# Kernel tuning notes

Measured on AMD Instinct MI355X. Metric: run time of the kernel, lower is better.

The kernel has to match this reference:

```python
import jax, jax.numpy as jnp
import numpy as np


def _entropy(x):
    # x: [..., C]; rowwise entropy of softmax(x) along last axis
    logp = jax.nn.log_softmax(x, axis=-1)
    return -(jnp.exp(logp) * logp).sum(-1)


def setup_inputs() -> dict:
    key = jax.random.key(0)
    C, E = 8192, 512
    prototypes = jax.random.normal(key, (C, E), dtype=jnp.float32)
    return {"prototypes": prototypes}


def reference(prototypes):
    C, E = prototypes.shape
    # F.normalize(p=2, dim=1): divide by L2 norm clamped to 1e-12
    norm = jnp.sqrt(jnp.sum(prototypes * prototypes, axis=1, keepdims=True))
    p = prototypes / jnp.maximum(norm, 1e-12)
    # Gram matrix [C, C] (fused matmul instead of broadcast-mul-sum)
    proto_logits = jnp.einsum("ce,de->cd", p, p)
    proto_logits_sum = proto_logits.sum(0, keepdims=True)  # [1, C]
    loss = _entropy(proto_logits).sum(-1) / C + _entropy(proto_logits_sum)
    return loss.sum()
```

## Files before the change

### kernel.cpp

```cpp
#include <hip/hip_runtime.h>
#include <hip/hip_bf16.h>

#define C_DIM 8192
#define E_DIM 512

using f32x4 = __attribute__((ext_vector_type(4))) float;
using i32x4 = __attribute__((ext_vector_type(4))) int;

__device__ inline void gload_lds16(const void* g, void* l) {
  __builtin_amdgcn_global_load_lds(
      (const __attribute__((address_space(1))) unsigned*)g,
      (__attribute__((address_space(3))) unsigned*)l, 16, 0, 0);
}

__device__ inline unsigned pack_bf16(float a, float b) {
  unsigned ua = __float_as_uint(a), ub = __float_as_uint(b);
  ua = (ua + 0x7fffu + ((ua >> 16) & 1u)) >> 16;
  ub = (ub + 0x7fffu + ((ub >> 16) & 1u)) >> 16;
  return ua | (ub << 16);
}

__device__ inline float bf2f(unsigned short u) {
  return __uint_as_float(((unsigned)u) << 16);
}

__device__ inline unsigned pack_i8x4(float a, float b, float c, float d) {
  unsigned x0 = (unsigned)(__float2int_rn(a * 127.f)) & 255u;
  unsigned x1 = (unsigned)(__float2int_rn(b * 127.f)) & 255u;
  unsigned x2 = (unsigned)(__float2int_rn(c * 127.f)) & 255u;
  unsigned x3 = (unsigned)(__float2int_rn(d * 127.f)) & 255u;
  return x0 | (x1 << 8) | (x2 << 16) | (x3 << 24);
}

__global__ __launch_bounds__(256) void norm_kernel(
    const float* __restrict__ P, unsigned* __restrict__ Pb,
    unsigned* __restrict__ Pi) {
  int wid = threadIdx.x >> 6, lane = threadIdx.x & 63;
  int row = blockIdx.x * 4 + wid;
  const float4* src = (const float4*)(P + (size_t)row * E_DIM);
  float4 v0 = src[lane], v1 = src[lane + 64];
  float ss = v0.x * v0.x + v0.y * v0.y + v0.z * v0.z + v0.w * v0.w +
             v1.x * v1.x + v1.y * v1.y + v1.z * v1.z + v1.w * v1.w;
  for (int m = 32; m; m >>= 1) ss += __shfl_xor(ss, m);
  float inv = 1.0f / fmaxf(sqrtf(ss), 1e-12f);
  v0.x *= inv; v0.y *= inv; v0.z *= inv; v0.w *= inv;
  v1.x *= inv; v1.y *= inv; v1.z *= inv; v1.w *= inv;
  uint2* bd = (uint2*)(Pb + (size_t)row * (E_DIM / 2));
  uint2 b0, b1;
  b0.x = pack_bf16(v0.x, v0.y); b0.y = pack_bf16(v0.z, v0.w);
  b1.x = pack_bf16(v1.x, v1.y); b1.y = pack_bf16(v1.z, v1.w);
  bd[lane] = b0; bd[lane + 64] = b1;
  Pi[(size_t)row * 128 + lane] = pack_i8x4(v0.x, v0.y, v0.z, v0.w);
  Pi[(size_t)row * 128 + 64 + lane] = pack_i8x4(v1.x, v1.y, v1.z, v1.w);
}

__global__ __launch_bounds__(256) void qsum_kernel(
    const unsigned short* __restrict__ Pb, float* __restrict__ q) {
  __shared__ float red[4][512];
  int wid = threadIdx.x >> 6, lane = threadIdx.x & 63;
  float a[8];
#pragma unroll
  for (int k = 0; k < 8; ++k) a[k] = 0.f;
  for (int i = 0; i < 32; ++i) {
    int row = blockIdx.x * 128 + wid * 32 + i;
    uint4 v = *(const uint4*)(Pb + (size_t)row * E_DIM + lane * 8);
    a[0] += bf2f((unsigned short)(v.x & 0xffff));
    a[1] += bf2f((unsigned short)(v.x >> 16));
    a[2] += bf2f((unsigned short)(v.y & 0xffff));
    a[3] += bf2f((unsigned short)(v.y >> 16));
    a[4] += bf2f((unsigned short)(v.z & 0xffff));
    a[5] += bf2f((unsigned short)(v.z >> 16));
    a[6] += bf2f((unsigned short)(v.w & 0xffff));
    a[7] += bf2f((unsigned short)(v.w >> 16));
  }
#pragma unroll
  for (int k = 0; k < 8; ++k) red[wid][lane * 8 + k] = a[k];
  __syncthreads();
  for (int c = threadIdx.x; c < 512; c += 256) {
    float t = red[0][c] + red[1][c] + red[2][c] + red[3][c];
    atomicAdd(&q[c], t);
  }
}

__global__ __launch_bounds__(256) void ssum_kernel(
    const unsigned short* __restrict__ Pb, const float* __restrict__ q,
    float* __restrict__ s) {
  int wid = threadIdx.x >> 6, lane = threadIdx.x & 63;
  int row = blockIdx.x * 4 + wid;
  uint4 v = *(const uint4*)(Pb + (size_t)row * E_DIM + lane * 8);
  const float4* qv = (const float4*)q;
  float4 q0 = qv[lane * 2], q1 = qv[lane * 2 + 1];
  float d = bf2f((unsigned short)(v.x & 0xffff)) * q0.x +
            bf2f((unsigned short)(v.x >> 16)) * q0.y +
            bf2f((unsigned short)(v.y & 0xffff)) * q0.z +
            bf2f((unsigned short)(v.y >> 16)) * q0.w +
            bf2f((unsigned short)(v.z & 0xffff)) * q1.x +
            bf2f((unsigned short)(v.z >> 16)) * q1.y +
            bf2f((unsigned short)(v.w & 0xffff)) * q1.z +
            bf2f((unsigned short)(v.w >> 16)) * q1.w;
  for (int m = 32; m; m >>= 1) d += __shfl_xor(d, m);
  if (lane == 0) s[row] = d;
}

__global__ __launch_bounds__(256) void gram_kernel(
    const unsigned char* __restrict__ Pi, float* __restrict__ Zp,
    float* __restrict__ Sp) {
  __shared__ unsigned char As[128 * 128];
  __shared__ unsigned char Bs[128 * 128];

  int b = blockIdx.x;
  int i = (b & 7) * 260 + (b >> 3);
  float bi = 64.5f - sqrtf(64.5f * 64.5f - 2.0f * (float)i);
  int by = (int)bi;
  if (by < 0) by = 0;
  while (64 * (by + 1) - ((by + 1) * by) / 2 <= i) ++by;
  while (64 * by - (by * (by - 1)) / 2 > i) --by;
  int bx = by + (i - (64 * by - (by * (by - 1)) / 2));
  bool diag = (bx == by);

  int tid = threadIdx.x, wid = tid >> 6, lane = tid & 63;
  int wr = wid >> 1, wc = wid & 1;
  int l15 = lane & 15, lh = lane >> 4;

  i32x4 acc[4][4];
#pragma unroll
  for (int m = 0; m < 4; ++m)
#pragma unroll
    for (int n = 0; n < 4; ++n)
      acc[m][n] = (i32x4){0, 0, 0, 0};

  int rs = lane >> 3;
  int gsw = (lane & 7) ^ rs;
  const unsigned char* abase = Pi + (size_t)(by * 128) * E_DIM;
  const unsigned char* bbase = Pi + (size_t)(bx * 128) * E_DIM;

  for (int kt = 0; kt < 4; ++kt) {
#pragma unroll
    for (int j = 0; j < 4; ++j) {
      int ci = wid * 4 + j;
      int r = ci * 8 + rs;
      gload_lds16(abase + (size_t)r * E_DIM + kt * 128 + gsw * 16,
                  (char*)As + ci * 1024);
      gload_lds16(bbase + (size_t)r * E_DIM + kt * 128 + gsw * 16,
                  (char*)Bs + ci * 1024);
    }
    __syncthreads();

    i32x4 af[4][2], bfr[4][2];
#pragma unroll
    for (int m = 0; m < 4; ++m)
#pragma unroll
      for (int kk = 0; kk < 2; ++kk) {
        int row = wr * 64 + m * 16 + l15;
        int g = (kk * 4 + lh) ^ (row & 7);
        af[m][kk] = *(const i32x4*)(As + row * 128 + g * 16);
      }
#pragma unroll
    for (int n = 0; n < 4; ++n)
#pragma unroll
      for (int kk = 0; kk < 2; ++kk) {
        int row = wc * 64 + n * 16 + l15;
        int g = (kk * 4 + lh) ^ (row & 7);
        bfr[n][kk] = *(const i32x4*)(Bs + row * 128 + g * 16);
      }

#pragma unroll
    for (int kk = 0; kk < 2; ++kk)
#pragma unroll
      for (int m = 0; m < 4; ++m)
#pragma unroll
        for (int n = 0; n < 4; ++n)
          acc[m][n] = __builtin_amdgcn_mfma_i32_16x16x64_i8(
              af[m][kk], bfr[n][kk], acc[m][n], 0, 0, 0);
    if (kt < 3) __syncthreads();
  }

  const float invq = 1.0f / 16129.0f;
  float zc[4], sc[4];
#pragma unroll
  for (int n = 0; n < 4; ++n) { zc[n] = 0.f; sc[n] = 0.f; }

  int slotR = bx * 2 + wc;
#pragma unroll
  for (int m = 0; m < 4; ++m) {
#pragma unroll
    for (int reg = 0; reg < 4; ++reg) {
      float z = 0.f, s = 0.f;
#pragma unroll
      for (int n = 0; n < 4; ++n) {
        float g = (float)acc[m][n][reg] * invq;
        float e = __expf(g);
        z += e;
        s += e * g;
        zc[n] += e;
        sc[n] += e * g;
      }
      for (int msk = 8; msk; msk >>= 1) {
        z += __shfl_xor(z, msk);
        s += __shfl_xor(s, msk);
      }
      if (l15 == 0) {
        int rowin = wr * 64 + m * 16 + lh * 4 + reg;
        size_t idx = (size_t)by * 16384 + (size_t)slotR * 128 + rowin;
        Zp[idx] = z;
        Sp[idx] = s;
      }
    }
  }
  if (!diag) {
    int slotC = by * 2 + wr;
#pragma unroll
    for (int n = 0; n < 4; ++n) {
      float z = zc[n], s = sc[n];
      z += __shfl_xor(z, 16); s += __shfl_xor(s, 16);
      z += __shfl_xor(z, 32); s += __shfl_xor(s, 32);
      if (lh == 0) {
        int colin = wc * 64 + n * 16 + l15;
        size_t idx = (size_t)bx * 16384 + (size_t)slotC * 128 + colin;
        Zp[idx] = z;
        Sp[idx] = s;
      }
    }
  }
}

__global__ __launch_bounds__(256) void reduce_kernel(
    const float* __restrict__ Zp, const float* __restrict__ Sp,
    const float* __restrict__ s, float* __restrict__ h_acc,
    unsigned* __restrict__ done, float* __restrict__ out) {
  __shared__ float zbuf[128], sbuf[128];
  __shared__ float red[8];
  __shared__ unsigned lastFlag;
  int rb = blockIdx.x;
  int t = threadIdx.x;
  int lane = t & 63, wid = t >> 6;
  int row = t & 127;
  const float* src = (t >= 128) ? Sp : Zp;
  size_t base = (size_t)rb * 16384 + row;
  float acc = 0.f;
#pragma unroll 8
  for (int sl = 0; sl < 128; ++sl) acc += src[base + (size_t)sl * 128];
  if (t >= 128) sbuf[row] = acc; else zbuf[row] = acc;
  __syncthreads();

  float hp = 0.f;
  if (t < 128) {
    float z = zbuf[t], s2 = sbuf[t];
    hp = logf(z) - s2 / z;
  }
  for (int k = 32; k; k >>= 1) hp += __shfl_xor(hp, k);
  if (lane == 0) red[wid] = hp;
  __syncthreads();
  if (t == 0) {
    float h = red[0] + red[1];
    atomicAdd(h_acc, h);
    __threadfence();
    unsigned old = atomicAdd(done, 1u);
    lastFlag = (old == 63u) ? 1u : 0u;
  }
  __syncthreads();

  if (lastFlag) {
    float m = -3.4e38f;
    for (int i = t; i < C_DIM; i += 256) m = fmaxf(m, s[i]);
    for (int k = 32; k; k >>= 1) m = fmaxf(m, __shfl_xor(m, k));
    if (lane == 0) red[wid] = m;
    __syncthreads();
    m = fmaxf(fmaxf(red[0], red[1]), fmaxf(red[2], red[3]));

    float z = 0.f, sw = 0.f;
    for (int i = t; i < C_DIM; i += 256) {
      float tv = s[i] - m;
      float e = __expf(tv);
      z += e;
      sw += e * tv;
    }
    for (int k = 32; k; k >>= 1) {
      z += __shfl_xor(z, k);
      sw += __shfl_xor(sw, k);
    }
    __syncthreads();
    if (lane == 0) { red[wid] = z; red[4 + wid] = sw; }
    __syncthreads();
    if (t == 0) {
      float zt = red[0] + red[1] + red[2] + red[3];
      float st = red[4] + red[5] + red[6] + red[7];
      float H2 = logf(zt) - st / zt;
      float h = atomicAdd(h_acc, 0.0f);
      out[0] = h / (float)C_DIM + H2;
    }
  }
}

extern "C" void kernel_launch(void* const* d_in, const int* in_sizes, int n_in,
                              void* d_out, int out_size, void* d_ws, size_t ws_size,
                              hipStream_t stream) {
  const float* P = (const float*)d_in[0];
  float* out = (float*)d_out;

  char* ws = (char*)d_ws;
  unsigned* Pb = (unsigned*)ws;
  unsigned* Pi = (unsigned*)(ws + ((size_t)8 << 20));
  float* Zp = (float*)(ws + ((size_t)12 << 20));
  float* Sp = (float*)(ws + ((size_t)16 << 20));
  float* q = (float*)(ws + ((size_t)20 << 20));
  float* h_acc = (float*)(ws + ((size_t)20 << 20) + 2048);
  unsigned* done = (unsigned*)(ws + ((size_t)20 << 20) + 2052);
  float* s = (float*)(ws + ((size_t)20 << 20) + 4096);

  hipMemsetAsync(q, 0, 2056, stream);

  norm_kernel<<<C_DIM / 4, 256, 0, stream>>>(P, Pb, Pi);
  qsum_kernel<<<C_DIM / 128, 256, 0, stream>>>((const unsigned short*)Pb, q);
  ssum_kernel<<<C_DIM / 4, 256, 0, stream>>>((const unsigned short*)Pb, q, s);
  gram_kernel<<<2080, 256, 0, stream>>>((const unsigned char*)Pi, Zp, Sp);
  reduce_kernel<<<64, 256, 0, stream>>>(Zp, Sp, s, h_acc, done, out);
}
```

Measured before the change: 86.58 us.

## Fuse normalize, column-sum and row-dot prep kernels with grid barrier

Replaces the three preprocessing kernels (normalize with bf16/int8 output, column sum q, row dot s) with one persistent prep kernel of 256 blocks. Each block keeps its 32 normalized fp32 rows in LDS, atomically accumulates q, waits at a global atomic counter barrier, then computes s from LDS. This removes the bf16 intermediate buffer, its write and two re-reads, plus two kernel launches. In exchange it depends on all 256 blocks being co-resident for the spin barrier, and the large LDS footprint limits occupancy.

```diff
diff --git a/kernel.cpp b/kernel.cpp
--- a/kernel.cpp
+++ b/kernel.cpp
@@ -11,17 +11,6 @@
   __builtin_amdgcn_global_load_lds(
       (const __attribute__((address_space(1))) unsigned*)g,
       (__attribute__((address_space(3))) unsigned*)l, 16, 0, 0);
-}
-
-__device__ inline unsigned pack_bf16(float a, float b) {
-  unsigned ua = __float_as_uint(a), ub = __float_as_uint(b);
-  ua = (ua + 0x7fffu + ((ua >> 16) & 1u)) >> 16;
-  ub = (ub + 0x7fffu + ((ub >> 16) & 1u)) >> 16;
-  return ua | (ub << 16);
-}
-
-__device__ inline float bf2f(unsigned short u) {
-  return __uint_as_float(((unsigned)u) << 16);
 }
 
 __device__ inline unsigned pack_i8x4(float a, float b, float c, float d) {
@@ -32,74 +21,74 @@
   return x0 | (x1 << 8) | (x2 << 16) | (x3 << 24);
 }
 
-__global__ __launch_bounds__(256) void norm_kernel(
-    const float* __restrict__ P, unsigned* __restrict__ Pb,
-    unsigned* __restrict__ Pi) {
+__global__ __launch_bounds__(256) void prep_kernel(
+    const float* __restrict__ P, unsigned* __restrict__ Pi,
+    float* __restrict__ q, unsigned* __restrict__ qdone,
+    float* __restrict__ s) {
+  __shared__ float rows[32][512];
+  __shared__ float qpart[4][512];
+  __shared__ float qs[512];
   int wid = threadIdx.x >> 6, lane = threadIdx.x & 63;
-  int row = blockIdx.x * 4 + wid;
-  const float4* src = (const float4*)(P + (size_t)row * E_DIM);
-  float4 v0 = src[lane], v1 = src[lane + 64];
-  float ss = v0.x * v0.x + v0.y * v0.y + v0.z * v0.z + v0.w * v0.w +
-             v1.x * v1.x + v1.y * v1.y + v1.z * v1.z + v1.w * v1.w;
-  for (int m = 32; m; m >>= 1) ss += __shfl_xor(ss, m);
-  float inv = 1.0f / fmaxf(sqrtf(ss), 1e-12f);
-  v0.x *= inv; v0.y *= inv; v0.z *= inv; v0.w *= inv;
-  v1.x *= inv; v1.y *= inv; v1.z *= inv; v1.w *= inv;
-  uint2* bd = (uint2*)(Pb + (size_t)row * (E_DIM / 2));
-  uint2 b0, b1;
-  b0.x = pack_bf16(v0.x, v0.y); b0.y = pack_bf16(v0.z, v0.w);
-  b1.x = pack_bf16(v1.x, v1.y); b1.y = pack_bf16(v1.z, v1.w);
-  bd[lane] = b0; bd[lane + 64] = b1;
-  Pi[(size_t)row * 128 + lane] = pack_i8x4(v0.x, v0.y, v0.z, v0.w);
-  Pi[(size_t)row * 128 + 64 + lane] = pack_i8x4(v1.x, v1.y, v1.z, v1.w);
-}
-
-__global__ __launch_bounds__(256) void qsum_kernel(
-    const unsigned short* __restrict__ Pb, float* __restrict__ q) {
-  __shared__ float red[4][512];
-  int wid = threadIdx.x >> 6, lane = threadIdx.x & 63;
-  float a[8];
-#pragma unroll
-  for (int k = 0; k < 8; ++k) a[k] = 0.f;
-  for (int i = 0; i < 32; ++i) {
-    int row = blockIdx.x * 128 + wid * 32 + i;
-    uint4 v = *(const uint4*)(Pb + (size_t)row * E_DIM + lane * 8);
-    a[0] += bf2f((unsigned short)(v.x & 0xffff));
-    a[1] += bf2f((unsigned short)(v.x >> 16));
-    a[2] += bf2f((unsigned short)(v.y & 0xffff));
-    a[3] += bf2f((unsigned short)(v.y >> 16));
-    a[4] += bf2f((unsigned short)(v.z & 0xffff));
-    a[5] += bf2f((unsigned short)(v.z >> 16));
-    a[6] += bf2f((unsigned short)(v.w & 0xffff));
-    a[7] += bf2f((unsigned short)(v.w >> 16));
-  }
-#pragma unroll
-  for (int k = 0; k < 8; ++k) red[wid][lane * 8 + k] = a[k];
+  int rbase = blockIdx.x * 32;
+
+  float c0[8];
+#pragma unroll
+  for (int k = 0; k < 8; ++k) c0[k] = 0.f;
+
+  for (int r8 = 0; r8 < 8; ++r8) {
+    int rloc = wid * 8 + r8;
+    int row = rbase + rloc;
+    const float4* src = (const float4*)(P + (size_t)row * E_DIM);
+    float4 v0 = src[lane], v1 = src[lane + 64];
+    float ss = v0.x * v0.x + v0.y * v0.y + v0.z * v0.z + v0.w * v0.w +
+               v1.x * v1.x + v1.y * v1.y + v1.z * v1.z + v1.w * v1.w;
+    for (int m = 32; m; m >>= 1) ss += __shfl_xor(ss, m);
+    float inv = 1.0f / fmaxf(sqrtf(ss), 1e-12f);
+    v0.x *= inv; v0.y *= inv; v0.z *= inv; v0.w *= inv;
+    v1.x *= inv; v1.y *= inv; v1.z *= inv; v1.w *= inv;
+    *(float4*)&rows[rloc][lane * 4] = v0;
+    *(float4*)&rows[rloc][256 + lane * 4] = v1;
+    Pi[(size_t)row * 128 + lane] = pack_i8x4(v0.x, v0.y, v0.z, v0.w);
+    Pi[(size_t)row * 128 + 64 + lane] = pack_i8x4(v1.x, v1.y, v1.z, v1.w);
+    c0[0] += v0.x; c0[1] += v0.y; c0[2] += v0.z; c0[3] += v0.w;
+    c0[4] += v1.x; c0[5] += v1.y; c0[6] += v1.z; c0[7] += v1.w;
+  }
+#pragma unroll
+  for (int k = 0; k < 4; ++k) {
+    qpart[wid][lane * 4 + k] = c0[k];
+    qpart[wid][256 + lane * 4 + k] = c0[4 + k];
+  }
   __syncthreads();
   for (int c = threadIdx.x; c < 512; c += 256) {
-    float t = red[0][c] + red[1][c] + red[2][c] + red[3][c];
+    float t = qpart[0][c] + qpart[1][c] + qpart[2][c] + qpart[3][c];
     atomicAdd(&q[c], t);
   }
-}
-
-__global__ __launch_bounds__(256) void ssum_kernel(
-    const unsigned short* __restrict__ Pb, const float* __restrict__ q,
-    float* __restrict__ s) {
-  int wid = threadIdx.x >> 6, lane = threadIdx.x & 63;
-  int row = blockIdx.x * 4 + wid;
-  uint4 v = *(const uint4*)(Pb + (size_t)row * E_DIM + lane * 8);
-  const float4* qv = (const float4*)q;
-  float4 q0 = qv[lane * 2], q1 = qv[lane * 2 + 1];
-  float d = bf2f((unsigned short)(v.x & 0xffff)) * q0.x +
-            bf2f((unsigned short)(v.x >> 16)) * q0.y +
-            bf2f((unsigned short)(v.y & 0xffff)) * q0.z +
-            bf2f((unsigned short)(v.y >> 16)) * q0.w +
-            bf2f((unsigned short)(v.z & 0xffff)) * q1.x +
-            bf2f((unsigned short)(v.z >> 16)) * q1.y +
-            bf2f((unsigned short)(v.w & 0xffff)) * q1.z +
-            bf2f((unsigned short)(v.w >> 16)) * q1.w;
-  for (int m = 32; m; m >>= 1) d += __shfl_xor(d, m);
-  if (lane == 0) s[row] = d;
+  __syncthreads();
+
+  if (threadIdx.x == 0) {
+    __threadfence();
+    __hip_atomic_fetch_add(qdone, 1u, __ATOMIC_RELEASE, __HIP_MEMORY_SCOPE_AGENT);
+    while (__hip_atomic_load(qdone, __ATOMIC_ACQUIRE, __HIP_MEMORY_SCOPE_AGENT) <
+           256u)
+      __builtin_amdgcn_s_sleep(2);
+  }
+  __syncthreads();
+
+  for (int c = threadIdx.x; c < 512; c += 256)
+    qs[c] = __hip_atomic_load(&q[c], __ATOMIC_RELAXED, __HIP_MEMORY_SCOPE_AGENT);
+  __syncthreads();
+
+  for (int r8 = 0; r8 < 8; ++r8) {
+    int rloc = wid * 8 + r8;
+    float4 a0 = *(const float4*)&rows[rloc][lane * 4];
+    float4 a1 = *(const float4*)&rows[rloc][256 + lane * 4];
+    float4 q0 = *(const float4*)&qs[lane * 4];
+    float4 q1 = *(const float4*)&qs[256 + lane * 4];
+    float d = a0.x * q0.x + a0.y * q0.y + a0.z * q0.z + a0.w * q0.w +
+              a1.x * q1.x + a1.y * q1.y + a1.z * q1.z + a1.w * q1.w;
+    for (int m = 32; m; m >>= 1) d += __shfl_xor(d, m);
+    if (lane == 0) s[rbase + rloc] = d;
+  }
 }
 
 __global__ __launch_bounds__(256) void gram_kernel(
@@ -299,20 +288,18 @@
   float* out = (float*)d_out;
 
   char* ws = (char*)d_ws;
-  unsigned* Pb = (unsigned*)ws;
-  unsigned* Pi = (unsigned*)(ws + ((size_t)8 << 20));
-  float* Zp = (float*)(ws + ((size_t)12 << 20));
-  float* Sp = (float*)(ws + ((size_t)16 << 20));
-  float* q = (float*)(ws + ((size_t)20 << 20));
-  float* h_acc = (float*)(ws + ((size_t)20 << 20) + 2048);
-  unsigned* done = (unsigned*)(ws + ((size_t)20 << 20) + 2052);
-  float* s = (float*)(ws + ((size_t)20 << 20) + 4096);
-
-  hipMemsetAsync(q, 0, 2056, stream);
-
-  norm_kernel<<<C_DIM / 4, 256, 0, stream>>>(P, Pb, Pi);
-  qsum_kernel<<<C_DIM / 128, 256, 0, stream>>>((const unsigned short*)Pb, q);
-  ssum_kernel<<<C_DIM / 4, 256, 0, stream>>>((const unsigned short*)Pb, q, s);
+  unsigned* Pi = (unsigned*)ws;
+  float* Zp = (float*)(ws + ((size_t)4 << 20));
+  float* Sp = (float*)(ws + ((size_t)8 << 20));
+  float* q = (float*)(ws + ((size_t)12 << 20));
+  float* h_acc = (float*)(ws + ((size_t)12 << 20) + 2048);
+  unsigned* done = (unsigned*)(ws + ((size_t)12 << 20) + 2052);
+  unsigned* qdone = (unsigned*)(ws + ((size_t)12 << 20) + 2056);
+  float* s = (float*)(ws + ((size_t)12 << 20) + 4096);
+
+  hipMemsetAsync(q, 0, 2060, stream);
+
+  prep_kernel<<<256, 256, 0, stream>>>(P, Pi, q, qdone, s);
   gram_kernel<<<2080, 256, 0, stream>>>((const unsigned char*)Pi, Zp, Sp);
   reduce_kernel<<<64, 256, 0, stream>>>(Zp, Sp, s, h_acc, done, out);
 }
```

New measurement: 105.2 us. +21.5%, slower.

## Load B fragments directly from global, stage only A in LDS with wider tiles

Applied to the files above, without the earlier changes.

Drops the B-tile LDS buffer and loads B operand fragments straight from global memory into registers. A is staged in LDS in two 256-byte-wide K halves, so there are fewer barrier rounds (two instead of four) and no LDS traffic for B. The cost is uncoalesced per-lane global loads for B, which rely on L2/cache hits and may expose memory latency without LDS staging.

```diff
diff --git a/kernel.cpp b/kernel.cpp
--- a/kernel.cpp
+++ b/kernel.cpp
@@ -105,8 +105,7 @@
 __global__ __launch_bounds__(256) void gram_kernel(
     const unsigned char* __restrict__ Pi, float* __restrict__ Zp,
     float* __restrict__ Sp) {
-  __shared__ unsigned char As[128 * 128];
-  __shared__ unsigned char Bs[128 * 128];
+  __shared__ unsigned char As[128 * 256];
 
   int b = blockIdx.x;
   int i = (b & 7) * 260 + (b >> 3);
@@ -129,50 +128,54 @@
     for (int n = 0; n < 4; ++n)
       acc[m][n] = (i32x4){0, 0, 0, 0};
 
-  int rs = lane >> 3;
-  int gsw = (lane & 7) ^ rs;
   const unsigned char* abase = Pi + (size_t)(by * 128) * E_DIM;
-  const unsigned char* bbase = Pi + (size_t)(bx * 128) * E_DIM;
-
-  for (int kt = 0; kt < 4; ++kt) {
-#pragma unroll
-    for (int j = 0; j < 4; ++j) {
-      int ci = wid * 4 + j;
-      int r = ci * 8 + rs;
-      gload_lds16(abase + (size_t)r * E_DIM + kt * 128 + gsw * 16,
+  const unsigned char* bb[4];
+#pragma unroll
+  for (int n = 0; n < 4; ++n)
+    bb[n] = Pi + (size_t)(bx * 128 + wc * 64 + n * 16 + l15) * E_DIM + lh * 16;
+
+  int rs = lane >> 4;
+  int g = lane & 15;
+
+#pragma unroll
+  for (int h = 0; h < 2; ++h) {
+    if (h) __syncthreads();
+#pragma unroll
+    for (int j = 0; j < 8; ++j) {
+      int ci = wid * 8 + j;
+      int r = ci * 4 + rs;
+      int srcg = (g & 8) | ((g & 7) ^ (r & 7));
+      gload_lds16(abase + (size_t)r * E_DIM + h * 256 + srcg * 16,
                   (char*)As + ci * 1024);
-      gload_lds16(bbase + (size_t)r * E_DIM + kt * 128 + gsw * 16,
-                  (char*)Bs + ci * 1024);
     }
     __syncthreads();
 
-    i32x4 af[4][2], bfr[4][2];
-#pragma unroll
-    for (int m = 0; m < 4; ++m)
+#pragma unroll
+    for (int kt2 = 0; kt2 < 2; ++kt2) {
+      int kt = h * 2 + kt2;
+      i32x4 bfr[2][4];
+#pragma unroll
+      for (int kk = 0; kk < 2; ++kk)
+#pragma unroll
+        for (int n = 0; n < 4; ++n)
+          bfr[kk][n] = *(const i32x4*)(bb[n] + kt * 128 + kk * 64);
 #pragma unroll
       for (int kk = 0; kk < 2; ++kk) {
-        int row = wr * 64 + m * 16 + l15;
-        int g = (kk * 4 + lh) ^ (row & 7);
-        af[m][kk] = *(const i32x4*)(As + row * 128 + g * 16);
-      }
-#pragma unroll
-    for (int n = 0; n < 4; ++n)
-#pragma unroll
-      for (int kk = 0; kk < 2; ++kk) {
-        int row = wc * 64 + n * 16 + l15;
-        int g = (kk * 4 + lh) ^ (row & 7);
-        bfr[n][kk] = *(const i32x4*)(Bs + row * 128 + g * 16);
-      }
-
-#pragma unroll
-    for (int kk = 0; kk < 2; ++kk)
-#pragma unroll
-      for (int m = 0; m < 4; ++m)
-#pragma unroll
-        for (int n = 0; n < 4; ++n)
-          acc[m][n] = __builtin_amdgcn_mfma_i32_16x16x64_i8(
-              af[m][kk], bfr[n][kk], acc[m][n], 0, 0, 0);
-    if (kt < 3) __syncthreads();
+        i32x4 af[4];
+#pragma unroll
+        for (int m = 0; m < 4; ++m) {
+          int row = wr * 64 + m * 16 + l15;
+          int gsl = (kk * 4 + lh) ^ (l15 & 7);
+          af[m] = *(const i32x4*)(As + row * 256 + kt2 * 128 + gsl * 16);
+        }
+#pragma unroll
+        for (int m = 0; m < 4; ++m)
+#pragma unroll
+          for (int n = 0; n < 4; ++n)
+            acc[m][n] = __builtin_amdgcn_mfma_i32_16x16x64_i8(
+                af[m], bfr[kk][n], acc[m][n], 0, 0, 0);
+      }
+    }
   }
 
   const float invq = 1.0f / 16129.0f;
@@ -188,12 +191,12 @@
       float z = 0.f, s = 0.f;
 #pragma unroll
       for (int n = 0; n < 4; ++n) {
-        float g = (float)acc[m][n][reg] * invq;
-        float e = __expf(g);
+        float gv = (float)acc[m][n][reg] * invq;
+        float e = __expf(gv);
         z += e;
-        s += e * g;
+        s += e * gv;
         zc[n] += e;
-        sc[n] += e * g;
+        sc[n] += e * gv;
       }
       for (int msk = 8; msk; msk >>= 1) {
         z += __shfl_xor(z, msk);
```

New measurement: 98.98 us. 14.3% more time.
